# Performance work log

Measured on AMD Instinct MI355X. Metric: run time of the kernel, lower is better.

## Reference

```python
import jax, jax.numpy as jnp
import numpy as np
import math

N_NODES = 50000
N_EDGES = 800000
IN_DIM = 128
OUT_DIM = 64
TIME_DIM = 128


def setup_inputs() -> dict:
    key = jax.random.key(0)
    ks = jax.random.split(key, 9)
    return {
        "node_feats": jax.random.normal(ks[0], (N_NODES, IN_DIM), dtype=jnp.float32),
        "time_diff": jax.random.uniform(ks[1], (N_EDGES,), dtype=jnp.float32),
        "src": jax.random.randint(ks[2], (N_EDGES,), 0, N_NODES, dtype=jnp.int32),
        "dst": jax.random.randint(ks[3], (N_EDGES,), 0, N_NODES, dtype=jnp.int32),
        "W": jax.random.normal(ks[4], (OUT_DIM, IN_DIM), dtype=jnp.float32) * 0.05,
        "Wv": jax.random.normal(ks[5], (OUT_DIM, IN_DIM), dtype=jnp.float32) * 0.05,
        "omega": jax.random.normal(ks[6], (TIME_DIM // 2,), dtype=jnp.float32),
        "Wt": jax.random.normal(ks[7], (OUT_DIM, TIME_DIM), dtype=jnp.float32) * 0.05,
        "a": jax.random.normal(ks[8], (3 * OUT_DIM,), dtype=jnp.float32) * 0.05,
    }


def reference(node_feats, time_diff, src, dst, W, Wv, omega, Wt, a):
    N = node_feats.shape[0]
    d = W.shape[0]  # out_dim
    time_dim = 2 * omega.shape[0]

    # gather + linear projections per edge
    h_src = node_feats[src] @ W.T          # [E, d]
    h_dst = node_feats[dst] @ W.T          # [E, d]
    v_src = node_feats[src] @ Wv.T         # [E, d]

    # temporal encoding: interleaved sin/cos of t * omega, scaled by sqrt(1/dim)
    ang = time_diff[:, None] * omega[None, :]                       # [E, dim/2]
    pe = jnp.stack([jnp.sin(ang), jnp.cos(ang)], axis=-1)
    pe = pe.reshape(ang.shape[0], time_dim) * jnp.float32(math.sqrt(1.0 / time_dim))
    t_emb = pe @ Wt.T                                               # [E, d]

    # attn_fc(concat([h_src, h_dst, t_emb])) == split dot products (same math, no big concat)
    e = h_src @ a[:d] + h_dst @ a[d:2 * d] + t_emb @ a[2 * d:]      # [E]
    e = jnp.where(e > 0, e, 0.2 * e)  # LeakyReLU(0.2)

    # edge_softmax: softmax over incoming edges of each destination node
    m = jax.ops.segment_max(e, dst, num_segments=N)
    ex = jnp.exp(e - m[dst])
    den = jax.ops.segment_sum(ex, dst, num_segments=N)
    alpha = ex / den[dst]  # dropout is identity in eval mode

    # weighted message scatter-sum aggregation
    msg = v_src * alpha[:, None]                                    # [E, d]
    return jax.ops.segment_sum(msg, dst, num_segments=N)            # [N, d]
```

## Files before the change

### kernel.cpp

```cpp
#include <hip/hip_runtime.h>
#include <hip/hip_bf16.h>
#include <hip/hip_fp16.h>
#include <math.h>

#define IN_DIM   128
#define OUT_DIM  64
#define THALF    64
#define PE_SCALE 0.08838834764831845f
#define TBL      2048
#define EPB_LOG  14
#define EPB      (1 << EPB_LOG)

typedef __attribute__((ext_vector_type(8))) short  short8;
typedef __attribute__((ext_vector_type(4))) float  f32x4;

__device__ inline unsigned short bf16_rne(float x) {
    unsigned u = __float_as_uint(x);
    return (unsigned short)((u + 0x7FFFu + ((u >> 16) & 1u)) >> 16);
}

__global__ __launch_bounds__(256) void k_prep(
    const float* __restrict__ W, const float* __restrict__ Wt,
    const float* __restrict__ a, const float* __restrict__ Wv,
    const float* __restrict__ omega,
    float* __restrict__ gtab, unsigned short* __restrict__ Bp,
    int* __restrict__ pref)
{
    __shared__ float satv[IN_DIM];
    __shared__ float saW1[IN_DIM], saW2[IN_DIM];
    int t = threadIdx.x;
    if (t < IN_DIM) {
        float x3 = 0.f;
        for (int j = 0; j < OUT_DIM; ++j)
            x3 += a[2 * OUT_DIM + j] * Wt[j * IN_DIM + t];
        satv[t] = x3;
        if (blockIdx.x == 0) {
            float x1 = 0.f, x2 = 0.f;
            for (int j = 0; j < OUT_DIM; ++j) {
                float wj = W[j * IN_DIM + t];
                x1 += a[j] * wj;
                x2 += a[OUT_DIM + j] * wj;
            }
            saW1[t] = x1; saW2[t] = x2;
        }
    }
    __syncthreads();

    int idx = blockIdx.x * 256 + t;
    if (idx <= TBL) {
        float tt = (float)idx * (1.0f / TBL);
        float acc = 0.f;
#pragma unroll
        for (int i = 0; i < THALF; ++i) {
            float sp, cp;
            __sincosf(tt * omega[i], &sp, &cp);
            acc += sp * satv[2 * i] + cp * satv[2 * i + 1];
        }
        gtab[idx] = acc;
    }
    if (idx < 64) pref[idx] = 0;

    if (blockIdx.x == 0) {
        for (int i = t; i < 5 * 4 * 64 * 8; i += 256) {
            int j    = i & 7;
            int lane = (i >> 3) & 63;
            int k0i  = (i >> 9) & 3;
            int tt   = i >> 11;
            int kk = k0i * 32 + (lane >> 4) * 8 + j;
            int n  = lane & 15;
            float val;
            if (tt < 4)     val = Wv[(tt * 16 + n) * IN_DIM + kk];
            else            val = (n == 0) ? saW1[kk] : (n == 1) ? saW2[kk] : 0.f;
            Bp[i] = bf16_rne(val);
        }
    }
}

__global__ __launch_bounds__(1024) void k_hist_mfma(
    const int* __restrict__ dst,
    unsigned short* __restrict__ lrank,
    unsigned short* __restrict__ ghist16,
    const float* __restrict__ feats,
    const unsigned short* __restrict__ Bp,
    unsigned short* __restrict__ vb,
    float* __restrict__ s1,
    float* __restrict__ s2,
    int N, int E, int B)
{
    extern __shared__ unsigned h[];
    int t = threadIdx.x;
    if ((int)blockIdx.x < B) {
        int NH = (N + 1) >> 1;
        for (int i = t; i < NH; i += 1024) h[i] = 0u;
        __syncthreads();
        int b = blockIdx.x;
        int e0 = b << EPB_LOG;
        int e1 = e0 + EPB; if (e1 > E) e1 = E;
        for (int e = e0 + t; e < e1; e += 1024) {
            int d = dst[e];
            unsigned inc = (d & 1) ? 0x10000u : 1u;
            unsigned old = atomicAdd(&h[d >> 1], inc);
            lrank[e] = (unsigned short)((d & 1) ? (old >> 16) : (old & 0xFFFFu));
        }
        __syncthreads();
        unsigned* gh32 = (unsigned*)(ghist16 + (size_t)b * N);
        for (int w = t; w < NH; w += 1024) gh32[w] = h[w];
        return;
    }
    int gwave = ((int)blockIdx.x - B) * 16 + (t >> 6);
    int lane  = t & 63;
    int ntiles = (N + 15) >> 4;
    if (gwave >= ntiles) return;
    int row = lane & 15, quad = lane >> 4;
    int nodeA = gwave * 16 + row;
    int nodeL = nodeA < N ? nodeA : N - 1;

    const float* arow = feats + (size_t)nodeL * IN_DIM + quad * 8;
    short8 afrag[4];
#pragma unroll
    for (int k0i = 0; k0i < 4; ++k0i) {
        float4 fa = *(const float4*)(arow + k0i * 32);
        float4 fb = *(const float4*)(arow + k0i * 32 + 4);
        union { unsigned u[4]; short8 s; } cv;
        cv.u[0] = (__float_as_uint(fa.x) >> 16) | (__float_as_uint(fa.y) & 0xFFFF0000u);
        cv.u[1] = (__float_as_uint(fa.z) >> 16) | (__float_as_uint(fa.w) & 0xFFFF0000u);
        cv.u[2] = (__float_as_uint(fb.x) >> 16) | (__float_as_uint(fb.y) & 0xFFFF0000u);
        cv.u[3] = (__float_as_uint(fb.z) >> 16) | (__float_as_uint(fb.w) & 0xFFFF0000u);
        afrag[k0i] = cv.s;
    }

    const short8* B8 = (const short8*)Bp;
    f32x4 acc[5];
#pragma unroll
    for (int tt = 0; tt < 5; ++tt) acc[tt] = (f32x4){0.f, 0.f, 0.f, 0.f};
#pragma unroll
    for (int tt = 0; tt < 5; ++tt) {
#pragma unroll
        for (int k0i = 0; k0i < 4; ++k0i)
            acc[tt] = __builtin_amdgcn_mfma_f32_16x16x32_bf16(
                afrag[k0i], B8[(tt * 4 + k0i) * 64 + lane], acc[tt], 0, 0, 0);
    }

    int col = lane & 15;
    int baseNode = gwave * 16 + quad * 4;
#pragma unroll
    for (int r = 0; r < 4; ++r) {
        int nd = baseNode + r;
        if (nd < N) {
            unsigned short* vr = vb + (size_t)nd * OUT_DIM + col;
#pragma unroll
            for (int tt = 0; tt < 4; ++tt) vr[tt * 16] = bf16_rne(acc[tt][r]);
            if (col == 0)      s1[nd] = acc[4][r];
            else if (col == 1) s2[nd] = acc[4][r];
        }
    }
}

__global__ __launch_bounds__(256) void k_scan_fuse(
    unsigned short* __restrict__ ghist16,
    int* __restrict__ offs,
    int* __restrict__ pref,
    int B, int N)
{
    __shared__ int lds[256];
    int b = blockIdx.x, t = threadIdx.x;
    int n0 = b * 1024 + t * 4;
    unsigned r0 = 0, r1 = 0, r2 = 0, r3 = 0;
    if (n0 + 3 < N) {
        for (int bb = 0; bb < B; ++bb) {
            unsigned short* p = ghist16 + (size_t)bb * N + n0;
            uint2 c = *(uint2*)p;
            uint2 w;
            w.x = (r0 & 0xFFFFu) | (r1 << 16);
            w.y = (r2 & 0xFFFFu) | (r3 << 16);
            *(uint2*)p = w;
            r0 += c.x & 0xFFFFu; r1 += c.x >> 16;
            r2 += c.y & 0xFFFFu; r3 += c.y >> 16;
        }
    } else if (n0 < N) {
        for (int bb = 0; bb < B; ++bb) {
            unsigned short* p = ghist16 + (size_t)bb * N + n0;
            unsigned c0 = p[0]; p[0] = (unsigned short)r0; r0 += c0;
            if (n0 + 1 < N) { unsigned c = p[1]; p[1] = (unsigned short)r1; r1 += c; }
            if (n0 + 2 < N) { unsigned c = p[2]; p[2] = (unsigned short)r2; r2 += c; }
            if (n0 + 3 < N) { unsigned c = p[3]; p[3] = (unsigned short)r3; r3 += c; }
        }
    }
    int s = (int)(r0 + r1 + r2 + r3);
    lds[t] = s;
    __syncthreads();
    for (int off = 1; off < 256; off <<= 1) {
        int tmp = (t >= off) ? lds[t - off] : 0;
        __syncthreads();
        lds[t] += tmp;
        __syncthreads();
    }
    int ex = lds[t] - s;
    if (n0 + 3 < N) {
        int4 o;
        o.x = ex;
        o.y = ex + (int)r0;
        o.z = ex + (int)(r0 + r1);
        o.w = ex + (int)(r0 + r1 + r2);
        *(int4*)(offs + n0) = o;
    } else if (n0 < N) {
        offs[n0] = ex;
        if (n0 + 1 < N) offs[n0 + 1] = ex + (int)r0;
        if (n0 + 2 < N) offs[n0 + 2] = ex + (int)(r0 + r1);
        if (n0 + 3 < N) offs[n0 + 3] = ex + (int)(r0 + r1 + r2);
    }
    int total = lds[255];
    if (t > b && t < (int)gridDim.x) atomicAdd(pref + t, total);
}

__global__ __launch_bounds__(256) void k_scatter_fused(
    const float* __restrict__ tdiff,
    const int* __restrict__ src,
    const int* __restrict__ dst,
    const float* __restrict__ gtab,
    const float* __restrict__ s1,
    const float* __restrict__ s2,
    const unsigned short* __restrict__ lrank,
    const unsigned short* __restrict__ ghist16,
    const int* __restrict__ offs,
    const int* __restrict__ pref,
    unsigned* __restrict__ payload,
    int N, int E)
{
    int base = (blockIdx.x * 256 + threadIdx.x) * 8;
    if (base >= E) return;
    if (base + 8 <= E) {
        int4   sa = *(const int4*)(src + base);
        int4   sb = *(const int4*)(src + base + 4);
        int4   da = *(const int4*)(dst + base);
        int4   db = *(const int4*)(dst + base + 4);
        float4 ta = *(const float4*)(tdiff + base);
        float4 tb = *(const float4*)(tdiff + base + 4);
        ushort4 la = *(const ushort4*)(lrank + base);
        ushort4 lb = *(const ushort4*)(lrank + base + 4);
        int s[8]    = {sa.x, sa.y, sa.z, sa.w, sb.x, sb.y, sb.z, sb.w};
        int d[8]    = {da.x, da.y, da.z, da.w, db.x, db.y, db.z, db.w};
        float tv[8] = {ta.x, ta.y, ta.z, ta.w, tb.x, tb.y, tb.z, tb.w};
        int lr[8]   = {la.x, la.y, la.z, la.w, lb.x, lb.y, lb.z, lb.w};

        int pos[8];
#pragma unroll
        for (int i = 0; i < 8; ++i) {
            int b = (base + i) >> EPB_LOG;
            pos[i] = offs[d[i]] + pref[d[i] >> 10] +
                     (int)ghist16[(size_t)b * N + d[i]] + lr[i];
        }
#pragma unroll
        for (int i = 0; i < 8; ++i) {
            float a1 = s1[s[i]];
            float a2 = s2[d[i]];
            float x = tv[i] * (float)TBL;
            int i0 = (int)x;
            i0 = i0 < 0 ? 0 : (i0 > TBL - 1 ? TBL - 1 : i0);
            float fr = x - (float)i0;
            float ev = a1 + a2 + PE_SCALE * (gtab[i0] + fr * (gtab[i0 + 1] - gtab[i0]));
            ev = ev > 0.f ? ev : 0.2f * ev;
            unsigned pw = ((unsigned)s[i] << 16) | (unsigned)__half_as_ushort(__float2half(ev));
            payload[pos[i]] = pw;
        }
    } else {
        for (int e = base; e < E; ++e) {
            int s = src[e], d = dst[e];
            float a1 = s1[s], a2 = s2[d];
            float x = tdiff[e] * (float)TBL;
            int i0 = (int)x;
            i0 = i0 < 0 ? 0 : (i0 > TBL - 1 ? TBL - 1 : i0);
            float fr = x - (float)i0;
            float ev = a1 + a2 + PE_SCALE * (gtab[i0] + fr * (gtab[i0 + 1] - gtab[i0]));
            ev = ev > 0.f ? ev : 0.2f * ev;
            unsigned pw = ((unsigned)s << 16) | (unsigned)__half_as_ushort(__float2half(ev));
            int b = e >> EPB_LOG;
            int pos = offs[d] + pref[d >> 10] + (int)ghist16[(size_t)b * N + d] + (int)lrank[e];
            payload[pos] = pw;
        }
    }
}

__global__ __launch_bounds__(256) void k_aggregate(
    const int* __restrict__ offs,
    const int* __restrict__ pref,
    const unsigned* __restrict__ payload,
    const unsigned short* __restrict__ vb,
    float* __restrict__ out,
    int N, int E)
{
    int wid  = (blockIdx.x * blockDim.x + threadIdx.x) >> 6;
    int lane = threadIdx.x & 63;
    if (wid >= N) return;
    int beg = offs[wid] + pref[wid >> 10];
    int end = (wid + 1 < N) ? (offs[wid + 1] + pref[(wid + 1) >> 10]) : E;
    int deg = end - beg;
    int g8 = lane >> 3, r = lane & 7;

    float acc[8];
#pragma unroll
    for (int i = 0; i < 8; ++i) acc[i] = 0.f;
    float den = 0.f;

    for (int base = 0; base < deg; base += 64) {
        int cl = deg - base; if (cl > 64) cl = 64;
        bool valid = lane < cl;
        unsigned pl = valid ? payload[beg + base + lane] : 0u;
        float ex = valid ? __expf(__half2float(__ushort_as_half((unsigned short)(pl & 0xFFFFu)))) : 0.f;
        int   sv = valid ? (int)(pl >> 16) : 0;

        int rounds = (cl + 15) >> 4;
        for (int j = 0; j < rounds; ++j) {
            int i0 = j * 16 + g8;
            int i1 = i0 + 8;
            float e0 = __shfl(ex, i0, 64);
            int   s0 = __shfl(sv, i0, 64);
            float e1 = __shfl(ex, i1, 64);
            int   s1v = __shfl(sv, i1, 64);
            den += e0 + e1;
            uint4 w0 = *((const uint4*)(vb + (size_t)s0 * OUT_DIM) + r);
            uint4 w1 = *((const uint4*)(vb + (size_t)s1v * OUT_DIM) + r);
            acc[0] += e0 * __uint_as_float(w0.x << 16)         + e1 * __uint_as_float(w1.x << 16);
            acc[1] += e0 * __uint_as_float(w0.x & 0xFFFF0000u) + e1 * __uint_as_float(w1.x & 0xFFFF0000u);
            acc[2] += e0 * __uint_as_float(w0.y << 16)         + e1 * __uint_as_float(w1.y << 16);
            acc[3] += e0 * __uint_as_float(w0.y & 0xFFFF0000u) + e1 * __uint_as_float(w1.y & 0xFFFF0000u);
            acc[4] += e0 * __uint_as_float(w0.z << 16)         + e1 * __uint_as_float(w1.z << 16);
            acc[5] += e0 * __uint_as_float(w0.z & 0xFFFF0000u) + e1 * __uint_as_float(w1.z & 0xFFFF0000u);
            acc[6] += e0 * __uint_as_float(w0.w << 16)         + e1 * __uint_as_float(w1.w << 16);
            acc[7] += e0 * __uint_as_float(w0.w & 0xFFFF0000u) + e1 * __uint_as_float(w1.w & 0xFFFF0000u);
        }
    }

#pragma unroll
    for (int i = 0; i < 8; ++i) {
        acc[i] += __shfl_xor(acc[i], 8, 64);
        acc[i] += __shfl_xor(acc[i], 16, 64);
        acc[i] += __shfl_xor(acc[i], 32, 64);
    }
    den += __shfl_xor(den, 8, 64);
    den += __shfl_xor(den, 16, 64);
    den += __shfl_xor(den, 32, 64);

    if (g8 == 0) {
        float inv = (deg > 0) ? 1.f / den : 0.f;
        float* o = out + (size_t)wid * OUT_DIM + r * 8;
        *(float4*)(o)     = make_float4(acc[0] * inv, acc[1] * inv, acc[2] * inv, acc[3] * inv);
        *(float4*)(o + 4) = make_float4(acc[4] * inv, acc[5] * inv, acc[6] * inv, acc[7] * inv);
    }
}

extern "C" void kernel_launch(void* const* d_in, const int* in_sizes, int n_in,
                              void* d_out, int out_size, void* d_ws, size_t ws_size,
                              hipStream_t stream) {
    const float* feats = (const float*)d_in[0];
    const float* tdiff = (const float*)d_in[1];
    const int*   src   = (const int*)d_in[2];
    const int*   dst   = (const int*)d_in[3];
    const float* W     = (const float*)d_in[4];
    const float* Wv    = (const float*)d_in[5];
    const float* omega = (const float*)d_in[6];
    const float* Wt    = (const float*)d_in[7];
    const float* a     = (const float*)d_in[8];
    float* out = (float*)d_out;

    int N = in_sizes[0] / IN_DIM;
    int E = in_sizes[1];
    int B = (E + EPB - 1) >> EPB_LOG;

    float* ws      = (float*)d_ws;
    unsigned short* vb = (unsigned short*)ws;
    float* s1      = ws + (size_t)N * 32;
    float* s2      = s1 + N;
    unsigned* payload = (unsigned*)(s2 + N);
    unsigned short* lrank = (unsigned short*)(payload + E);
    int*   offs    = (int*)(lrank + ((E + 1) & ~1));
    int    offs_elems = ((N + 1023) / 1024) * 1024;
    int*   pref    = offs + offs_elems;
    float* gtab    = (float*)(pref + 64);
    unsigned short* Bp = (unsigned short*)(gtab + TBL + 1);
    size_t gho = ((size_t)((char*)(Bp + 10240) - (char*)ws) + 7) & ~(size_t)7;
    unsigned short* ghist16 = (unsigned short*)((char*)ws + gho);

    int nb = (N + 1023) / 1024;
    int ntiles = (N + 15) / 16;
    int mblocks = (ntiles + 15) / 16;
    int eb8 = (E + 8 * 256 - 1) / (8 * 256);
    unsigned ldsb = (unsigned)(((N + 1) / 2) * 4);

    k_prep<<<(TBL / 256) + 1, 256, 0, stream>>>(W, Wt, a, Wv, omega, gtab, Bp, pref);
    k_hist_mfma<<<B + mblocks, 1024, ldsb, stream>>>(dst, lrank, ghist16,
                                                     feats, Bp, vb, s1, s2, N, E, B);
    k_scan_fuse<<<nb, 256, 0, stream>>>(ghist16, offs, pref, B, N);
    k_scatter_fused<<<eb8, 256, 0, stream>>>(tdiff, src, dst, gtab, s1, s2,
                                             lrank, ghist16, offs, pref, payload, N, E);
    long long tot = (long long)N * OUT_DIM;
    k_aggregate<<<(int)((tot + 255) / 256), 256, 0, stream>>>(offs, pref, payload, vb, out, N, E);
}
```

Baseline: 174.8 us.

## Aggregate each node with 16 threads instead of a full wavefront

Reworks the aggregation kernel so each destination node is handled by a 16-lane group instead of a 64-lane wavefront. Each lane owns 4 output features, walks the node's edge list directly and prefetches the next two payload words, which removes the cross-lane shuffles and the final xor reductions. With an average in-degree of about 16, the old mapping left many lanes idle per node. The cost is redundant payload loads and exp evaluations across the 16 lanes, and a sequential per-edge loop with less memory-level parallelism for high-degree nodes.

Measured after the change: 172.2 us. About the same (-1.5%).

```diff
diff --git a/kernel.cpp b/kernel.cpp
--- a/kernel.cpp
+++ b/kernel.cpp
@@ -289,64 +289,38 @@
     float* __restrict__ out,
     int N, int E)
 {
-    int wid  = (blockIdx.x * blockDim.x + threadIdx.x) >> 6;
-    int lane = threadIdx.x & 63;
-    if (wid >= N) return;
-    int beg = offs[wid] + pref[wid >> 10];
-    int end = (wid + 1 < N) ? (offs[wid + 1] + pref[(wid + 1) >> 10]) : E;
+    int gid  = blockIdx.x * 256 + threadIdx.x;
+    int node = gid >> 4;
+    int l16  = gid & 15;
+    if (node >= N) return;
+    int beg = offs[node] + pref[node >> 10];
+    int end = (node + 1 < N) ? (offs[node + 1] + pref[(node + 1) >> 10]) : E;
     int deg = end - beg;
-    int g8 = lane >> 3, r = lane & 7;
-
-    float acc[8];
-#pragma unroll
-    for (int i = 0; i < 8; ++i) acc[i] = 0.f;
-    float den = 0.f;
-
-    for (int base = 0; base < deg; base += 64) {
-        int cl = deg - base; if (cl > 64) cl = 64;
-        bool valid = lane < cl;
-        unsigned pl = valid ? payload[beg + base + lane] : 0u;
-        float ex = valid ? __expf(__half2float(__ushort_as_half((unsigned short)(pl & 0xFFFFu)))) : 0.f;
-        int   sv = valid ? (int)(pl >> 16) : 0;
-
-        int rounds = (cl + 15) >> 4;
-        for (int j = 0; j < rounds; ++j) {
-            int i0 = j * 16 + g8;
-            int i1 = i0 + 8;
-            float e0 = __shfl(ex, i0, 64);
-            int   s0 = __shfl(sv, i0, 64);
-            float e1 = __shfl(ex, i1, 64);
-            int   s1v = __shfl(sv, i1, 64);
-            den += e0 + e1;
-            uint4 w0 = *((const uint4*)(vb + (size_t)s0 * OUT_DIM) + r);
-            uint4 w1 = *((const uint4*)(vb + (size_t)s1v * OUT_DIM) + r);
-            acc[0] += e0 * __uint_as_float(w0.x << 16)         + e1 * __uint_as_float(w1.x << 16);
-            acc[1] += e0 * __uint_as_float(w0.x & 0xFFFF0000u) + e1 * __uint_as_float(w1.x & 0xFFFF0000u);
-            acc[2] += e0 * __uint_as_float(w0.y << 16)         + e1 * __uint_as_float(w1.y << 16);
-            acc[3] += e0 * __uint_as_float(w0.y & 0xFFFF0000u) + e1 * __uint_as_float(w1.y & 0xFFFF0000u);
-            acc[4] += e0 * __uint_as_float(w0.z << 16)         + e1 * __uint_as_float(w1.z << 16);
-            acc[5] += e0 * __uint_as_float(w0.z & 0xFFFF0000u) + e1 * __uint_as_float(w1.z & 0xFFFF0000u);
-            acc[6] += e0 * __uint_as_float(w0.w << 16)         + e1 * __uint_as_float(w1.w << 16);
-            acc[7] += e0 * __uint_as_float(w0.w & 0xFFFF0000u) + e1 * __uint_as_float(w1.w & 0xFFFF0000u);
-        }
-    }
-
-#pragma unroll
-    for (int i = 0; i < 8; ++i) {
-        acc[i] += __shfl_xor(acc[i], 8, 64);
-        acc[i] += __shfl_xor(acc[i], 16, 64);
-        acc[i] += __shfl_xor(acc[i], 32, 64);
-    }
-    den += __shfl_xor(den, 8, 64);
-    den += __shfl_xor(den, 16, 64);
-    den += __shfl_xor(den, 32, 64);
-
-    if (g8 == 0) {
-        float inv = (deg > 0) ? 1.f / den : 0.f;
-        float* o = out + (size_t)wid * OUT_DIM + r * 8;
-        *(float4*)(o)     = make_float4(acc[0] * inv, acc[1] * inv, acc[2] * inv, acc[3] * inv);
-        *(float4*)(o + 4) = make_float4(acc[4] * inv, acc[5] * inv, acc[6] * inv, acc[7] * inv);
-    }
+
+    float acc0 = 0.f, acc1 = 0.f, acc2 = 0.f, acc3 = 0.f, den = 0.f;
+    unsigned plA = (deg > 0) ? payload[beg] : 0u;
+    unsigned plB = (deg > 1) ? payload[beg + 1] : 0u;
+    for (int j = 0; j < deg; j += 2) {
+        unsigned pl0 = plA, pl1 = plB;
+        bool v1 = (j + 1 < deg);
+        if (j + 2 < deg) plA = payload[beg + j + 2];
+        if (j + 3 < deg) plB = payload[beg + j + 3];
+        float ex0 = __expf(__half2float(__ushort_as_half((unsigned short)(pl0 & 0xFFFFu))));
+        float ex1 = v1 ? __expf(__half2float(__ushort_as_half((unsigned short)(pl1 & 0xFFFFu)))) : 0.f;
+        int sv0 = (int)(pl0 >> 16);
+        int sv1 = v1 ? (int)(pl1 >> 16) : 0;
+        uint2 w0 = *(const uint2*)(vb + (size_t)sv0 * OUT_DIM + l16 * 4);
+        uint2 w1 = *(const uint2*)(vb + (size_t)sv1 * OUT_DIM + l16 * 4);
+        den  += ex0 + ex1;
+        acc0 += ex0 * __uint_as_float(w0.x << 16)         + ex1 * __uint_as_float(w1.x << 16);
+        acc1 += ex0 * __uint_as_float(w0.x & 0xFFFF0000u) + ex1 * __uint_as_float(w1.x & 0xFFFF0000u);
+        acc2 += ex0 * __uint_as_float(w0.y << 16)         + ex1 * __uint_as_float(w1.y << 16);
+        acc3 += ex0 * __uint_as_float(w0.y & 0xFFFF0000u) + ex1 * __uint_as_float(w1.y & 0xFFFF0000u);
+    }
+
+    float inv = (deg > 0) ? 1.f / den : 0.f;
+    float* o = out + (size_t)node * OUT_DIM + l16 * 4;
+    *(float4*)o = make_float4(acc0 * inv, acc1 * inv, acc2 * inv, acc3 * inv);
 }
 
 extern "C" void kernel_launch(void* const* d_in, const int* in_sizes, int n_in,
@@ -393,6 +367,6 @@
     k_scan_fuse<<<nb, 256, 0, stream>>>(ghist16, offs, pref, B, N);
     k_scatter_fused<<<eb8, 256, 0, stream>>>(tdiff, src, dst, gtab, s1, s2,
                                              lrank, ghist16, offs, pref, payload, N, E);
-    long long tot = (long long)N * OUT_DIM;
-    k_aggregate<<<(int)((tot + 255) / 256), 256, 0, stream>>>(offs, pref, payload, vb, out, N, E);
-}
+    long long aggt = (long long)N * 16;
+    k_aggregate<<<(int)((aggt + 255) / 256), 256, 0, stream>>>(offs, pref, payload, vb, out, N, E);
+}
```
